# Kernel tuning notes

Measured on AMD Instinct MI355X. Metric: run time of the kernel, lower is better.

The kernel has to match this reference:

```python
import jax, jax.numpy as jnp
import numpy as np

N_NODES = 50000
N_EDGES = 800000
IN_X = 64
IN_E = 32
HID = 64
NUM_GRAPHS = 50
EPS = 1e-5


def setup_inputs() -> dict:
    key = jax.random.key(0)
    ks = jax.random.split(key, 16)
    x = jax.random.normal(ks[0], (N_NODES, IN_X), dtype=jnp.float32)
    edge_index = jax.random.randint(ks[1], (2, N_EDGES), 0, N_NODES, dtype=jnp.int32)
    edge_attr = jax.random.normal(ks[2], (N_EDGES, IN_E), dtype=jnp.float32)
    batch = jnp.sort(jax.random.randint(ks[3], (N_NODES,), 0, NUM_GRAPHS, dtype=jnp.int32))
    s1 = 1.0 / np.sqrt(IN_X + IN_E)
    s2 = 1.0 / np.sqrt(HID + IN_E)
    sr = 1.0 / np.sqrt(IN_X)
    sh = 1.0 / np.sqrt(HID)
    return {
        "x": x, "edge_index": edge_index, "edge_attr": edge_attr, "batch": batch,
        "Wn1": jax.random.uniform(ks[4], (IN_X + IN_E, HID), jnp.float32, -s1, s1),
        "bn1": jax.random.uniform(ks[5], (HID,), jnp.float32, -s1, s1),
        "Wr1": jax.random.uniform(ks[6], (IN_X, HID), jnp.float32, -sr, sr),
        "g1": jnp.ones((HID,), jnp.float32), "be1": jnp.zeros((HID,), jnp.float32),
        "Wn2": jax.random.uniform(ks[7], (HID + IN_E, HID), jnp.float32, -s2, s2),
        "bn2": jax.random.uniform(ks[8], (HID,), jnp.float32, -s2, s2),
        "Wr2": jax.random.uniform(ks[9], (HID, HID), jnp.float32, -sh, sh),
        "g2": jnp.ones((HID,), jnp.float32), "be2": jnp.zeros((HID,), jnp.float32),
        "Wro": jax.random.uniform(ks[10], (HID, 1), jnp.float32, -sh, sh),
        "bro": jax.random.uniform(ks[11], (1,), jnp.float32, -sh, sh),
    }


def _edge_sage_conv(x, src, dst, edge_attr, Wn, bn, Wr):
    # message: concat(x_j, edge_attr) -> linear -> relu  (per-edge, [E, hid])
    m = jax.nn.relu(jnp.concatenate([x[src], edge_attr], axis=-1) @ Wn + bn)
    # scatter-mean onto destination nodes
    s = jax.ops.segment_sum(m, dst, num_segments=N_NODES)
    cnt = jax.ops.segment_sum(jnp.ones((dst.shape[0],), m.dtype), dst, num_segments=N_NODES)
    aggr = s / jnp.maximum(cnt, 1.0)[:, None]
    return x @ Wr + aggr


def _batchnorm(x, gamma, beta):
    mu = jnp.mean(x, axis=0)
    var = jnp.mean(jnp.square(x - mu), axis=0)  # biased var, training-mode BN
    return gamma * (x - mu) * jax.lax.rsqrt(var + EPS) + beta


def reference(x, edge_index, edge_attr, batch, Wn1, bn1, Wr1, g1, be1,
              Wn2, bn2, Wr2, g2, be2, Wro, bro):
    src, dst = edge_index[0], edge_index[1]
    h = _edge_sage_conv(x, src, dst, edge_attr, Wn1, bn1, Wr1)
    h = jax.nn.relu(_batchnorm(h, g1, be1))
    h = _edge_sage_conv(h, src, dst, edge_attr, Wn2, bn2, Wr2)
    h = jax.nn.relu(_batchnorm(h, g2, be2))
    # global mean pool per graph
    s = jax.ops.segment_sum(h, batch, num_segments=NUM_GRAPHS)
    cnt = jax.ops.segment_sum(jnp.ones((h.shape[0],), h.dtype), batch, num_segments=NUM_GRAPHS)
    hg = s / jnp.maximum(cnt, 1.0)[:, None]
    return (hg @ Wro + bro).squeeze(-1)
```

## Files before the change

### kernel.cpp

```cpp
#include <hip/hip_runtime.h>

#define N_NODES   50000
#define N_EDGES   800000
#define HID       64
#define NUM_GRAPHS 50
#define EPS       1e-5f
#define NB_COMBINE 256
#define NHPAD     50176
#define SCAN_B    98
#define NBKT      98
#define BSH       9
#define BATCH     2048

typedef __attribute__((ext_vector_type(8))) short short8;
typedef __attribute__((ext_vector_type(4))) float f32x4;

__device__ __forceinline__ unsigned short bfbits(float x) {
    __bf16 h = (__bf16)x;
    return __builtin_bit_cast(unsigned short, h);
}
__device__ __forceinline__ short8 cvt8hi(const float4& a, const float4& b) {
    float f[8] = {a.x, a.y, a.z, a.w, b.x, b.y, b.z, b.w};
    short8 hi;
#pragma unroll
    for (int i = 0; i < 8; ++i) hi[i] = (short)bfbits(f[i]);
    return hi;
}

__global__ __launch_bounds__(256) void k_hist(const int* __restrict__ dst,
                                              int* __restrict__ ihist) {
    int tid = blockIdx.x * blockDim.x + threadIdx.x;
    int stride = gridDim.x * blockDim.x;
    for (int e = tid; e < N_EDGES; e += stride) atomicAdd(&ihist[dst[e]], 1);
}

__global__ __launch_bounds__(512) void k_scan1(const int* __restrict__ ihist,
                                               int* __restrict__ off,
                                               int* __restrict__ bsum) {
    __shared__ int s[512];
    const int t = threadIdx.x, i = blockIdx.x * 512 + t;
    const int v = ihist[i];
    s[t] = v;
    __syncthreads();
    for (int o = 1; o < 512; o <<= 1) {
        int u = (t >= o) ? s[t - o] : 0;
        __syncthreads();
        s[t] += u;
        __syncthreads();
    }
    off[i] = s[t] - v;
    if (t == 511) bsum[blockIdx.x] = s[t];
}

__global__ void k_scan2(const int* __restrict__ bsum, int* __restrict__ bscan) {
    if (threadIdx.x == 0) {
        int acc = 0;
        for (int b = 0; b < SCAN_B; ++b) { bscan[b] = acc; acc += bsum[b]; }
    }
}

__global__ __launch_bounds__(512) void k_scan3(int* __restrict__ off,
                                               const int* __restrict__ bscan) {
    const int i = blockIdx.x * 512 + threadIdx.x;
    off[i] += bscan[i >> 9];
}

__global__ void k_bcur(const int* __restrict__ off, int* __restrict__ bcur) {
    int b = threadIdx.x;
    if (b < NBKT) bcur[b] = off[b << BSH];
}

__global__ __launch_bounds__(256) void k_bin(const int* __restrict__ src,
                                             const int* __restrict__ dst,
                                             int* __restrict__ bcur,
                                             int2* __restrict__ binned) {
    __shared__ int bh[NBKT], gb[NBKT];
    const int tid = threadIdx.x;
    const int base = blockIdx.x * BATCH + tid * 8;
    int2 rec[8]; int bk[8]; bool val[8];
#pragma unroll
    for (int j = 0; j < 8; ++j) {
        const int e = base + j;
        val[j] = e < N_EDGES;
        if (val[j]) {
            const int d = dst[e];
            rec[j] = int2{src[e] | (d << 16), e};
            bk[j] = d >> BSH;
        } else bk[j] = 0;
    }
    if (tid < NBKT) bh[tid] = 0;
    __syncthreads();
#pragma unroll
    for (int j = 0; j < 8; ++j) if (val[j]) atomicAdd(&bh[bk[j]], 1);
    __syncthreads();
    if (tid < NBKT) { gb[tid] = atomicAdd(&bcur[tid], bh[tid]); bh[tid] = 0; }
    __syncthreads();
#pragma unroll
    for (int j = 0; j < 8; ++j)
        if (val[j]) {
            const int r = atomicAdd(&bh[bk[j]], 1);
            binned[gb[bk[j]] + r] = rec[j];
        }
}

__global__ __launch_bounds__(256) void k_sortb(const int2* __restrict__ binned,
                                               const int* __restrict__ off,
                                               int2* __restrict__ epk) {
    __shared__ int cur[512];
    const int b = blockIdx.x;
    const int nbase = b << BSH;
    const int tid = threadIdx.x;
    for (int i = tid; i < 512; i += 256) cur[i] = off[nbase + i];
    const int start = off[nbase];
    const int end = (b == NBKT - 1) ? N_EDGES : off[nbase + 512];
    __syncthreads();
    for (int p = start + tid; p < end; p += 256) {
        const int2 r = binned[p];
        const int d = ((unsigned)r.x) >> 16;
        const int pos = atomicAdd(&cur[d - nbase], 1);
        epk[pos] = r;
    }
}

__global__ __launch_bounds__(256) void k_prepEA(const float* __restrict__ ea,
                                                unsigned short* __restrict__ eaB) {
    int t = blockIdx.x * blockDim.x + threadIdx.x;
    if (t >= N_EDGES * 4) return;
    float4 a = *(const float4*)(ea + (size_t)t * 8);
    float4 b = *(const float4*)(ea + (size_t)t * 8 + 4);
    *(short8*)(eaB + (size_t)t * 8) = cvt8hi(a, b);
}

__global__ void k_gcnt(const int* __restrict__ batch, float* __restrict__ gcnt) {
    int g = threadIdx.x;
    if (g >= NUM_GRAPHS) return;
    auto lb = [&](int val) {
        int lo = 0, hi = N_NODES;
        while (lo < hi) { int mid = (lo + hi) >> 1; if (batch[mid] < val) lo = mid + 1; else hi = mid; }
        return lo;
    };
    gcnt[g] = (float)(lb(g + 1) - lb(g));
}

__global__ void k_prepW(const float* __restrict__ W, unsigned short* __restrict__ Wb) {
    int t = blockIdx.x * blockDim.x + threadIdx.x;
    if (t >= 96 * 64) return;
    int k = t >> 6, n = t & 63;
    Wb[n * 104 + k] = bfbits(W[t]);
}

__global__ __launch_bounds__(256) void k_prepX(const float* __restrict__ x,
                                               unsigned short* __restrict__ xb) {
    int t = blockIdx.x * blockDim.x + threadIdx.x;
    if (t >= N_NODES * 8) return;
    float4 a = ((const float4*)(x + (size_t)t * 8))[0];
    float4 b = ((const float4*)(x + (size_t)t * 8))[1];
    *(short8*)(xb + (size_t)t * 8) = cvt8hi(a, b);
}

__global__ __launch_bounds__(256) void k_prepH(const float* __restrict__ h,
                                               const float* __restrict__ ss,
                                               float* __restrict__ hn,
                                               unsigned short* __restrict__ hb) {
    int t = blockIdx.x * blockDim.x + threadIdx.x;
    if (t >= N_NODES * 8) return;
    const int f0 = (t & 7) * 8;
    float4 sca = *(const float4*)(ss + f0);
    float4 scb = *(const float4*)(ss + f0 + 4);
    float4 sha = *(const float4*)(ss + 64 + f0);
    float4 shb = *(const float4*)(ss + 64 + f0 + 4);
    const float* r = h + (size_t)t * 8;
    float4 a = ((const float4*)r)[0];
    float4 b = ((const float4*)r)[1];
    a.x = fmaxf(a.x * sca.x + sha.x, 0.f);
    a.y = fmaxf(a.y * sca.y + sha.y, 0.f);
    a.z = fmaxf(a.z * sca.z + sha.z, 0.f);
    a.w = fmaxf(a.w * sca.w + sha.w, 0.f);
    b.x = fmaxf(b.x * scb.x + shb.x, 0.f);
    b.y = fmaxf(b.y * scb.y + shb.y, 0.f);
    b.z = fmaxf(b.z * scb.z + shb.z, 0.f);
    b.w = fmaxf(b.w * scb.w + shb.w, 0.f);
    ((float4*)(hn + (size_t)t * 8))[0] = a;
    ((float4*)(hn + (size_t)t * 8))[1] = b;
    *(short8*)(hb + (size_t)t * 8) = cvt8hi(a, b);
}

__global__ __launch_bounds__(256) void k_edge(const unsigned short* __restrict__ xb,
                                              const unsigned short* __restrict__ eaB,
                                              const int2* __restrict__ epk,
                                              const unsigned short* __restrict__ Wb,
                                              const float* __restrict__ bias,
                                              float* __restrict__ aggr) {
    __shared__ int ldstw[4][2][16];

    const int tid  = threadIdx.x;
    const int lane = tid & 63;
    const int w    = tid >> 6;
    const int ew   = (blockIdx.x * 4 + w) * 32;

    const int fr   = lane & 15;
    const int hi4  = lane >> 4;
    const int koff = hi4 * 8;
    const int rb   = hi4 * 4;

    if (lane < 32)
        ldstw[w][lane >> 4][lane & 15] = ((unsigned)epk[ew + lane].x) >> 16;

    const int2 eA = epk[ew + fr];
    const int2 eB = epk[ew + 16 + fr];
    const int sA = eA.x & 0xffff, iA = eA.y;
    const int sB = eB.x & 0xffff, iB = eB.y;

    short8 aA0 = *(const short8*)(xb + (size_t)sA * 64 + koff);
    short8 aA1 = *(const short8*)(xb + (size_t)sA * 64 + 32 + koff);
    short8 aA2 = *(const short8*)(eaB + (size_t)iA * 32 + koff);
    short8 aB0 = *(const short8*)(xb + (size_t)sB * 64 + koff);
    short8 aB1 = *(const short8*)(xb + (size_t)sB * 64 + 32 + koff);
    short8 aB2 = *(const short8*)(eaB + (size_t)iB * 32 + koff);

    f32x4 accA[4], accB[4];
#pragma unroll
    for (int n = 0; n < 4; ++n) {
        const float bv = bias[n * 16 + fr];
        accA[n] = f32x4{bv, bv, bv, bv};
        accB[n] = f32x4{bv, bv, bv, bv};
    }

#pragma unroll
    for (int kb = 0; kb < 3; ++kb) {
        const short8 aA = (kb == 0) ? aA0 : (kb == 1) ? aA1 : aA2;
        const short8 aB = (kb == 0) ? aB0 : (kb == 1) ? aB1 : aB2;
#pragma unroll
        for (int nn = 0; nn < 4; ++nn) {
            const short8 bh = *(const short8*)(Wb + (nn * 16 + fr) * 104 + kb * 32 + koff);
            accA[nn] = __builtin_amdgcn_mfma_f32_16x16x32_bf16(aA, bh, accA[nn], 0, 0, 0);
            accB[nn] = __builtin_amdgcn_mfma_f32_16x16x32_bf16(aB, bh, accB[nn], 0, 0, 0);
        }
    }

#pragma unroll
    for (int n = 0; n < 4; ++n)
#pragma unroll
        for (int j = 0; j < 4; ++j) {
            accA[n][j] = fmaxf(accA[n][j], 0.f);
            accB[n][j] = fmaxf(accB[n][j], 0.f);
        }

#define SEGREDUCE(TT, ACC)                                                    \
    {                                                                         \
        int r = 0;                                                            \
        while (r < 16) {                                                      \
            const int d = ldstw[w][TT][r];                                    \
            int e2 = r + 1;                                                   \
            while (e2 < 16 && ldstw[w][TT][e2] == d) ++e2;                    \
            float v0 = 0.f, v1 = 0.f, v2 = 0.f, v3 = 0.f;                     \
            _Pragma("unroll")                                                 \
            for (int j = 0; j < 4; ++j) {                                     \
                const bool in = (rb + j >= r) && (rb + j < e2);               \
                v0 += in ? ACC[0][j] : 0.f;                                   \
                v1 += in ? ACC[1][j] : 0.f;                                   \
                v2 += in ? ACC[2][j] : 0.f;                                   \
                v3 += in ? ACC[3][j] : 0.f;                                   \
            }                                                                 \
            v0 += __shfl_xor(v0, 16); v0 += __shfl_xor(v0, 32);               \
            v1 += __shfl_xor(v1, 16); v1 += __shfl_xor(v1, 32);               \
            v2 += __shfl_xor(v2, 16); v2 += __shfl_xor(v2, 32);               \
            v3 += __shfl_xor(v3, 16); v3 += __shfl_xor(v3, 32);               \
            const float val = hi4 == 0 ? v0 : hi4 == 1 ? v1 : hi4 == 2 ? v2 : v3; \
            unsafeAtomicAdd(&aggr[(size_t)d * 64 + lane], val);               \
            r = e2;                                                           \
        }                                                                     \
    }
    SEGREDUCE(0, accA)
    SEGREDUCE(1, accB)
#undef SEGREDUCE
}

__global__ __launch_bounds__(256) void k_combine(const float* __restrict__ xin,
                                                 const float* __restrict__ Wr,
                                                 const float* __restrict__ aggr,
                                                 const int*   __restrict__ ihist,
                                                 float* __restrict__ h,
                                                 float* __restrict__ partial) {
    const int lane = threadIdx.x & 63;
    const int wv   = threadIdx.x >> 6;
    const int wid  = (blockIdx.x * blockDim.x + threadIdx.x) >> 6;
    const int nw   = (gridDim.x * blockDim.x) >> 6;

    float w[64];
#pragma unroll
    for (int k = 0; k < 64; ++k) w[k] = Wr[k * 64 + lane];

    float rs = 0.f, rq = 0.f;
    for (int n = wid; n < N_NODES; n += nw) {
        const float* __restrict__ xr = xin + (size_t)n * 64;
        const float c = fmaxf((float)ihist[n], 1.0f);
        float acc = aggr[(size_t)n * 64 + lane] / c;
#pragma unroll
        for (int k = 0; k < 64; ++k) acc += xr[k] * w[k];
        h[(size_t)n * 64 + lane] = acc;
        rs += acc;
        rq += acc * acc;
    }
    __shared__ float ssum[4][64];
    __shared__ float ssq[4][64];
    ssum[wv][lane] = rs;
    ssq[wv][lane]  = rq;
    __syncthreads();
    if (threadIdx.x < 64) {
        float s = ssum[0][lane] + ssum[1][lane] + ssum[2][lane] + ssum[3][lane];
        partial[blockIdx.x * 128 + lane] = s;
    } else if (threadIdx.x < 128) {
        int l = threadIdx.x - 64;
        float q = ssq[0][l] + ssq[1][l] + ssq[2][l] + ssq[3][l];
        partial[blockIdx.x * 128 + 64 + l] = q;
    }
}

__global__ void k_bnfin(const float* __restrict__ partial, const float* __restrict__ g,
                        const float* __restrict__ be, float* __restrict__ ss) {
    __shared__ float tot[128];
    int t = threadIdx.x;
    float s = 0.f;
    for (int b = 0; b < NB_COMBINE; ++b) s += partial[b * 128 + t];
    tot[t] = s;
    __syncthreads();
    if (t < 64) {
        float mu  = tot[t] * (1.0f / (float)N_NODES);
        float var = tot[64 + t] * (1.0f / (float)N_NODES) - mu * mu;
        float sc  = g[t] * rsqrtf(var + EPS);
        ss[t]      = sc;
        ss[64 + t] = be[t] - mu * sc;
    }
}

__global__ __launch_bounds__(256) void k_bnpool(const float* __restrict__ h,
                                                const float* __restrict__ ss,
                                                const int* __restrict__ batch,
                                                float* __restrict__ gsum) {
    const int lane = threadIdx.x & 63;
    const int wid  = (blockIdx.x * blockDim.x + threadIdx.x) >> 6;
    const int nw   = (gridDim.x * blockDim.x) >> 6;
    const float sc = ss[lane];
    const float sh = ss[64 + lane];
    const int chunk = (N_NODES + nw - 1) / nw;
    const int n0 = wid * chunk;
    const int n1 = min(n0 + chunk, N_NODES);
    int curg = -1;
    float acc = 0.f;
    for (int n = n0; n < n1; ++n) {
        int g = __builtin_amdgcn_readfirstlane(batch[n]);
        if (g != curg) {
            if (curg >= 0) unsafeAtomicAdd(&gsum[curg * 64 + lane], acc);
            curg = g;
            acc = 0.f;
        }
        acc += fmaxf(h[(size_t)n * 64 + lane] * sc + sh, 0.f);
    }
    if (curg >= 0) unsafeAtomicAdd(&gsum[curg * 64 + lane], acc);
}

__global__ void k_final(const float* __restrict__ gsum, const float* __restrict__ gcnt,
                        const float* __restrict__ Wro, const float* __restrict__ bro,
                        float* __restrict__ out) {
    int g = blockIdx.x;
    int lane = threadIdx.x;
    float v = gsum[g * 64 + lane] / fmaxf(gcnt[g], 1.0f) * Wro[lane];
#pragma unroll
    for (int off = 32; off > 0; off >>= 1) v += __shfl_down(v, off, 64);
    if (lane == 0) out[g] = v + bro[0];
}

extern "C" void kernel_launch(void* const* d_in, const int* in_sizes, int n_in,
                              void* d_out, int out_size, void* d_ws, size_t ws_size,
                              hipStream_t stream) {
    (void)in_sizes; (void)n_in; (void)out_size; (void)ws_size;
    const float* x    = (const float*)d_in[0];
    const int*   ei   = (const int*)d_in[1];
    const float* ea   = (const float*)d_in[2];
    const int*   batch= (const int*)d_in[3];
    const float* Wn1  = (const float*)d_in[4];
    const float* bn1  = (const float*)d_in[5];
    const float* Wr1  = (const float*)d_in[6];
    const float* g1   = (const float*)d_in[7];
    const float* be1  = (const float*)d_in[8];
    const float* Wn2  = (const float*)d_in[9];
    const float* bn2  = (const float*)d_in[10];
    const float* Wr2  = (const float*)d_in[11];
    const float* g2   = (const float*)d_in[12];
    const float* be2  = (const float*)d_in[13];
    const float* Wro  = (const float*)d_in[14];
    const float* bro  = (const float*)d_in[15];
    const int* src = ei;
    const int* dst = ei + N_EDGES;

    float* ws = (float*)d_ws;
    float* gsum   = ws;
    float* aggr   = gsum + 3200;
    int*   ihist  = (int*)(aggr + (size_t)N_NODES * 64);
    const size_t zero_floats = 3200 + (size_t)N_NODES * 64 + NHPAD;
    float* h      = (float*)(ihist + NHPAD);
    float* hn     = h + (size_t)N_NODES * 64;
    float* gcnt   = hn + (size_t)N_NODES * 64;
    float* part1  = gcnt + 64;
    float* part2  = part1 + NB_COMBINE * 128;
    float* ss1    = part2 + NB_COMBINE * 128;
    float* ss2    = ss1 + 128;
    unsigned short* Wb1 = (unsigned short*)(ss2 + 128);
    unsigned short* Wb2 = Wb1 + 6656;
    int* off     = (int*)(Wb2 + 6656);
    int* bsum    = off + NHPAD;
    int* bscan   = bsum + 128;
    int* bcur    = bscan + 128;
    int2* epk    = (int2*)(bcur + 128);
    int2* binned = epk + N_EDGES;
    unsigned short* xb  = (unsigned short*)(binned + N_EDGES);
    unsigned short* hb  = xb + (size_t)N_NODES * 64;
    unsigned short* eaB = hb + (size_t)N_NODES * 64;

    hipMemsetAsync(d_ws, 0, zero_floats * sizeof(float), stream);

    k_hist<<<512, 256, 0, stream>>>(dst, ihist);
    k_scan1<<<SCAN_B, 512, 0, stream>>>(ihist, off, bsum);
    k_scan2<<<1, 64, 0, stream>>>(bsum, bscan);
    k_scan3<<<SCAN_B, 512, 0, stream>>>(off, bscan);
    k_bcur<<<1, 128, 0, stream>>>(off, bcur);
    k_bin<<<(N_EDGES + BATCH - 1) / BATCH, 256, 0, stream>>>(src, dst, bcur, binned);
    k_sortb<<<NBKT, 256, 0, stream>>>(binned, off, epk);
    k_prepEA<<<N_EDGES * 4 / 256, 256, 0, stream>>>(ea, eaB);

    k_gcnt<<<1, 64, 0, stream>>>(batch, gcnt);
    k_prepW<<<24, 256, 0, stream>>>(Wn1, Wb1);
    k_prepW<<<24, 256, 0, stream>>>(Wn2, Wb2);
    k_prepX<<<(N_NODES * 8 + 255) / 256, 256, 0, stream>>>(x, xb);

    k_edge<<<N_EDGES / 128, 256, 0, stream>>>(xb, eaB, epk, Wb1, bn1, aggr);
    k_combine<<<NB_COMBINE, 256, 0, stream>>>(x, Wr1, aggr, ihist, h, part1);
    k_bnfin<<<1, 128, 0, stream>>>(part1, g1, be1, ss1);
    k_prepH<<<(N_NODES * 8 + 255) / 256, 256, 0, stream>>>(h, ss1, hn, hb);

    hipMemsetAsync(aggr, 0, (size_t)N_NODES * 64 * sizeof(float), stream);
    k_edge<<<N_EDGES / 128, 256, 0, stream>>>(hb, eaB, epk, Wb2, bn2, aggr);
    k_combine<<<NB_COMBINE, 256, 0, stream>>>(hn, Wr2, aggr, ihist, h, part2);
    k_bnfin<<<1, 128, 0, stream>>>(part2, g2, be2, ss2);

    k_bnpool<<<256, 256, 0, stream>>>(h, ss2, batch, gsum);
    k_final<<<NUM_GRAPHS, 64, 0, stream>>>(gsum, gcnt, Wro, bro, (float*)d_out);
}
```

Baseline: 379.6 us.

## Compute root linear in combine with bf16 MFMA and drop fp32 hn buffer

Replaces the scalar fp32 per-lane dot product in k_combine with bf16 MFMA 16x16x32 tiles. It reads the bf16 node features already produced for the edge kernel and a pre-transposed bf16 copy of Wr. This removes the fp32 hn write in prepH and its reread, and cuts ALU work in combine. The cost is that the root term now uses bf16 precision, and bnfin must reduce over more partial blocks.

```diff
diff --git a/kernel.cpp b/kernel.cpp
--- a/kernel.cpp
+++ b/kernel.cpp
@@ -5,7 +5,8 @@
 #define HID       64
 #define NUM_GRAPHS 50
 #define EPS       1e-5f
-#define NB_COMBINE 256
+#define NWT       3125
+#define NBC       782
 #define NHPAD     50176
 #define SCAN_B    98
 #define NBKT      98
@@ -149,6 +150,13 @@
     Wb[n * 104 + k] = bfbits(W[t]);
 }
 
+__global__ void k_prepWr(const float* __restrict__ Wr, unsigned short* __restrict__ Wrb) {
+    int t = blockIdx.x * blockDim.x + threadIdx.x;
+    if (t >= 64 * 64) return;
+    int k = t >> 6, n = t & 63;
+    Wrb[n * 64 + k] = bfbits(Wr[t]);
+}
+
 __global__ __launch_bounds__(256) void k_prepX(const float* __restrict__ x,
                                                unsigned short* __restrict__ xb) {
     int t = blockIdx.x * blockDim.x + threadIdx.x;
@@ -160,7 +168,6 @@
 
 __global__ __launch_bounds__(256) void k_prepH(const float* __restrict__ h,
                                                const float* __restrict__ ss,
-                                               float* __restrict__ hn,
                                                unsigned short* __restrict__ hb) {
     int t = blockIdx.x * blockDim.x + threadIdx.x;
     if (t >= N_NODES * 8) return;
@@ -180,8 +187,6 @@
     b.y = fmaxf(b.y * scb.y + shb.y, 0.f);
     b.z = fmaxf(b.z * scb.z + shb.z, 0.f);
     b.w = fmaxf(b.w * scb.w + shb.w, 0.f);
-    ((float4*)(hn + (size_t)t * 8))[0] = a;
-    ((float4*)(hn + (size_t)t * 8))[1] = b;
     *(short8*)(hb + (size_t)t * 8) = cvt8hi(a, b);
 }
 
@@ -276,44 +281,77 @@
 #undef SEGREDUCE
 }
 
-__global__ __launch_bounds__(256) void k_combine(const float* __restrict__ xin,
-                                                 const float* __restrict__ Wr,
+__global__ __launch_bounds__(256) void k_combine(const unsigned short* __restrict__ xbin,
+                                                 const unsigned short* __restrict__ Wrb,
                                                  const float* __restrict__ aggr,
                                                  const int*   __restrict__ ihist,
                                                  float* __restrict__ h,
                                                  float* __restrict__ partial) {
-    const int lane = threadIdx.x & 63;
-    const int wv   = threadIdx.x >> 6;
-    const int wid  = (blockIdx.x * blockDim.x + threadIdx.x) >> 6;
-    const int nw   = (gridDim.x * blockDim.x) >> 6;
-
-    float w[64];
-#pragma unroll
-    for (int k = 0; k < 64; ++k) w[k] = Wr[k * 64 + lane];
-
-    float rs = 0.f, rq = 0.f;
-    for (int n = wid; n < N_NODES; n += nw) {
-        const float* __restrict__ xr = xin + (size_t)n * 64;
-        const float c = fmaxf((float)ihist[n], 1.0f);
-        float acc = aggr[(size_t)n * 64 + lane] / c;
-#pragma unroll
-        for (int k = 0; k < 64; ++k) acc += xr[k] * w[k];
-        h[(size_t)n * 64 + lane] = acc;
-        rs += acc;
-        rq += acc * acc;
-    }
     __shared__ float ssum[4][64];
     __shared__ float ssq[4][64];
-    ssum[wv][lane] = rs;
-    ssq[wv][lane]  = rq;
-    __syncthreads();
-    if (threadIdx.x < 64) {
-        float s = ssum[0][lane] + ssum[1][lane] + ssum[2][lane] + ssum[3][lane];
-        partial[blockIdx.x * 128 + lane] = s;
-    } else if (threadIdx.x < 128) {
-        int l = threadIdx.x - 64;
-        float q = ssq[0][l] + ssq[1][l] + ssq[2][l] + ssq[3][l];
-        partial[blockIdx.x * 128 + 64 + l] = q;
+
+    const int tid  = threadIdx.x;
+    const int lane = tid & 63;
+    const int w    = tid >> 6;
+    const int wt   = blockIdx.x * 4 + w;
+    const int fr   = lane & 15;
+    const int hi4  = lane >> 4;
+    const int koff = hi4 * 8;
+    const int rb   = hi4 * 4;
+
+    float rs[4] = {0.f, 0.f, 0.f, 0.f};
+    float rq[4] = {0.f, 0.f, 0.f, 0.f};
+
+    if (wt < NWT) {
+        const int n0 = wt * 16;
+        const short8 a0 = *(const short8*)(xbin + (size_t)(n0 + fr) * 64 + koff);
+        const short8 a1 = *(const short8*)(xbin + (size_t)(n0 + fr) * 64 + 32 + koff);
+        f32x4 acc[4] = {};
+#pragma unroll
+        for (int kb = 0; kb < 2; ++kb) {
+            const short8 a = kb == 0 ? a0 : a1;
+#pragma unroll
+            for (int nn = 0; nn < 4; ++nn) {
+                const short8 bh = *(const short8*)(Wrb + (nn * 16 + fr) * 64 + kb * 32 + koff);
+                acc[nn] = __builtin_amdgcn_mfma_f32_16x16x32_bf16(a, bh, acc[nn], 0, 0, 0);
+            }
+        }
+        const int4 degs = *(const int4*)(ihist + n0 + rb);
+#pragma unroll
+        for (int j = 0; j < 4; ++j) {
+            const int dg = (&degs.x)[j];
+            const float invc = 1.0f / fmaxf((float)dg, 1.0f);
+            const int row = n0 + rb + j;
+#pragma unroll
+            for (int nn = 0; nn < 4; ++nn) {
+                const float v = acc[nn][j] + aggr[(size_t)row * 64 + nn * 16 + fr] * invc;
+                h[(size_t)row * 64 + nn * 16 + fr] = v;
+                rs[nn] += v;
+                rq[nn] += v * v;
+            }
+        }
+    }
+
+#pragma unroll
+    for (int nn = 0; nn < 4; ++nn) {
+        rs[nn] += __shfl_xor(rs[nn], 16); rs[nn] += __shfl_xor(rs[nn], 32);
+        rq[nn] += __shfl_xor(rq[nn], 16); rq[nn] += __shfl_xor(rq[nn], 32);
+    }
+    if (hi4 == 0) {
+#pragma unroll
+        for (int nn = 0; nn < 4; ++nn) {
+            ssum[w][nn * 16 + fr] = rs[nn];
+            ssq[w][nn * 16 + fr]  = rq[nn];
+        }
+    }
+    __syncthreads();
+    if (tid < 64) {
+        partial[blockIdx.x * 128 + tid] =
+            ssum[0][tid] + ssum[1][tid] + ssum[2][tid] + ssum[3][tid];
+    } else if (tid < 128) {
+        int l = tid - 64;
+        partial[blockIdx.x * 128 + 64 + l] =
+            ssq[0][l] + ssq[1][l] + ssq[2][l] + ssq[3][l];
     }
 }
 
@@ -322,7 +360,7 @@
     __shared__ float tot[128];
     int t = threadIdx.x;
     float s = 0.f;
-    for (int b = 0; b < NB_COMBINE; ++b) s += partial[b * 128 + t];
+    for (int b = 0; b < NBC; ++b) s += partial[b * 128 + t];
     tot[t] = s;
     __syncthreads();
     if (t < 64) {
@@ -400,15 +438,16 @@
     int*   ihist  = (int*)(aggr + (size_t)N_NODES * 64);
     const size_t zero_floats = 3200 + (size_t)N_NODES * 64 + NHPAD;
     float* h      = (float*)(ihist + NHPAD);
-    float* hn     = h + (size_t)N_NODES * 64;
-    float* gcnt   = hn + (size_t)N_NODES * 64;
+    float* gcnt   = h + (size_t)N_NODES * 64;
     float* part1  = gcnt + 64;
-    float* part2  = part1 + NB_COMBINE * 128;
-    float* ss1    = part2 + NB_COMBINE * 128;
+    float* part2  = part1 + NBC * 128;
+    float* ss1    = part2 + NBC * 128;
     float* ss2    = ss1 + 128;
-    unsigned short* Wb1 = (unsigned short*)(ss2 + 128);
-    unsigned short* Wb2 = Wb1 + 6656;
-    int* off     = (int*)(Wb2 + 6656);
+    unsigned short* Wb1  = (unsigned short*)(ss2 + 128);
+    unsigned short* Wb2  = Wb1 + 6656;
+    unsigned short* Wrb1 = Wb2 + 6656;
+    unsigned short* Wrb2 = Wrb1 + 4096;
+    int* off     = (int*)(Wrb2 + 4096);
     int* bsum    = off + NHPAD;
     int* bscan   = bsum + 128;
     int* bcur    = bscan + 128;
@@ -432,16 +471,18 @@
     k_gcnt<<<1, 64, 0, stream>>>(batch, gcnt);
     k_prepW<<<24, 256, 0, stream>>>(Wn1, Wb1);
     k_prepW<<<24, 256, 0, stream>>>(Wn2, Wb2);
+    k_prepWr<<<16, 256, 0, stream>>>(Wr1, Wrb1);
+    k_prepWr<<<16, 256, 0, stream>>>(Wr2, Wrb2);
     k_prepX<<<(N_NODES * 8 + 255) / 256, 256, 0, stream>>>(x, xb);
 
     k_edge<<<N_EDGES / 128, 256, 0, stream>>>(xb, eaB, epk, Wb1, bn1, aggr);
-    k_combine<<<NB_COMBINE, 256, 0, stream>>>(x, Wr1, aggr, ihist, h, part1);
+    k_combine<<<NBC, 256, 0, stream>>>(xb, Wrb1, aggr, ihist, h, part1);
     k_bnfin<<<1, 128, 0, stream>>>(part1, g1, be1, ss1);
-    k_prepH<<<(N_NODES * 8 + 255) / 256, 256, 0, stream>>>(h, ss1, hn, hb);
+    k_prepH<<<(N_NODES * 8 + 255) / 256, 256, 0, stream>>>(h, ss1, hb);
 
     hipMemsetAsync(aggr, 0, (size_t)N_NODES * 64 * sizeof(float), stream);
     k_edge<<<N_EDGES / 128, 256, 0, stream>>>(hb, eaB, epk, Wb2, bn2, aggr);
-    k_combine<<<NB_COMBINE, 256, 0, stream>>>(hn, Wr2, aggr, ihist, h, part2);
+    k_combine<<<NBC, 256, 0, stream>>>(hb, Wrb2, aggr, ihist, h, part2);
     k_bnfin<<<1, 128, 0, stream>>>(part2, g2, be2, ss2);
 
     k_bnpool<<<256, 256, 0, stream>>>(h, ss2, batch, gsum);
```

New measurement: 315.4 us. 16.9% less time.
